# Kernel optimization log

Measured on AMD Instinct MI355X. Metric: run time of the kernel, lower is better.

The kernel has to match this reference:

```python
import jax, jax.numpy as jnp
import numpy as np

MARGIN = 0.25


def _cdist(x, y):
    # Euclidean distance matrix, same math as torch.cdist(p=2).
    # x: [M, D], y: [K, D] -> [M, K]
    sq = (
        jnp.sum(x * x, axis=1, keepdims=True)
        + jnp.sum(y * y, axis=1)[None, :]
        - 2.0 * (x @ y.T)
    )
    return jnp.sqrt(jnp.maximum(sq, 0.0))


def setup_inputs() -> dict:
    key = jax.random.key(0)
    k1, k2, k3 = jax.random.split(key, 3)
    B, P, N, D = 2048, 2048, 16, 128
    anchor = jax.random.normal(k1, (B, D), dtype=jnp.float32)
    positive = jax.random.normal(k2, (P, D), dtype=jnp.float32)
    negative = jax.random.normal(k3, (B, N, D), dtype=jnp.float32)
    return {"anchor": anchor, "positive": positive, "negative": negative}


def reference(anchor, positive, negative):
    B, N, D = negative.shape
    # hardest positive: max distance to any positive, per anchor -> [B]
    d_pos = _cdist(anchor, positive).max(axis=1)
    # Original torch code expands negatives across a redundant batch dim and
    # takes min over the flattened (B*B*N); per row this equals the GLOBAL min
    # over all anchor-negative pairs. Compute it without the duplication.
    neg_flat = negative.reshape(B * N, D)  # [B*N, D]
    d_neg = _cdist(anchor, neg_flat).min()  # scalar
    losses = jax.nn.relu(d_pos - d_neg + MARGIN)  # [B]
    return losses.mean()
```

## Files before the change

kernel.cpp:

```cpp
#include <hip/hip_runtime.h>
#include <hip/hip_bf16.h>

#define MARGIN_F 0.25f

#define B_ANCH 2048
#define P_POS  2048
#define N_NEG  32768
#define DDIM   128

typedef __attribute__((ext_vector_type(8))) short bf16x8;
typedef __attribute__((ext_vector_type(4))) float f32x4;

__device__ __forceinline__ short f2bf(float x) {
    __hip_bfloat16 h = __float2bfloat16(x);
    return *reinterpret_cast<short*>(&h);
}

__global__ __launch_bounds__(256) void prep_kernel(
    const float* __restrict__ anchor, const float* __restrict__ positive,
    const float* __restrict__ negative,
    short* __restrict__ pA, short* __restrict__ pP, short* __restrict__ pN,
    float* __restrict__ nA, float* __restrict__ nP, float* __restrict__ nN,
    unsigned* __restrict__ dposBits, unsigned* __restrict__ dnegBits)
{
    const int tile = blockIdx.x * 4 + (threadIdx.x >> 6);
    const int lane = threadIdx.x & 63;
    const int lm = lane & 15, lk = lane >> 4;

    const float* src; short* dst; float* nrm; int t;
    const int TA = B_ANCH / 16, TP = P_POS / 16;
    if (tile < TA) {
        src = anchor; dst = pA; nrm = nA; t = tile;
        if (lm == lane) dposBits[tile * 16 + lm] = 0u;
    } else if (tile < TA + TP) {
        src = positive; dst = pP; nrm = nP; t = tile - TA;
    } else {
        src = negative; dst = pN; nrm = nN; t = tile - TA - TP;
    }
    if (blockIdx.x == 0 && threadIdx.x == 0) *dnegBits = 0x7F800000u;

    const int row = t * 16 + lm;
    float ss = 0.f;
    #pragma unroll
    for (int s = 0; s < 4; ++s) {
        const float* sp = src + (size_t)row * DDIM + s * 32 + lk * 8;
        float4 v0 = *(const float4*)sp;
        float4 v1 = *(const float4*)(sp + 4);
        ss += v0.x*v0.x + v0.y*v0.y + v0.z*v0.z + v0.w*v0.w
            + v1.x*v1.x + v1.y*v1.y + v1.z*v1.z + v1.w*v1.w;
        bf16x8 o;
        o[0]=f2bf(v0.x); o[1]=f2bf(v0.y); o[2]=f2bf(v0.z); o[3]=f2bf(v0.w);
        o[4]=f2bf(v1.x); o[5]=f2bf(v1.y); o[6]=f2bf(v1.z); o[7]=f2bf(v1.w);
        *(bf16x8*)(dst + ((size_t)(t * 4 + s) * 64 + lane) * 8) = o;
    }
    ss += __shfl_xor(ss, 16);
    ss += __shfl_xor(ss, 32);
    if (lk == 0) nrm[row] = ss;
}

template<int MODE, int CT>
__device__ __forceinline__ void dist_tile(
    const bf16x8* __restrict__ Af, const bf16x8* __restrict__ Yf,
    const float* __restrict__ nA, const float* __restrict__ nY,
    int by, int bx,
    unsigned* __restrict__ dposBits, unsigned* __restrict__ dnegBits)
{
    const int wid  = threadIdx.x >> 6;
    const int lane = threadIdx.x & 63;
    const int lm = lane & 15, lk = lane >> 4;
    const int wr = wid >> 1, wc = wid & 1;
    const int rt0 = by * 8 + wr * 4;

    bf16x8 a[4][4];
    #pragma unroll
    for (int m = 0; m < 4; ++m)
        #pragma unroll
        for (int s = 0; s < 4; ++s)
            a[m][s] = Af[(size_t)((rt0 + m) * 4 + s) * 64 + lane];

    float red[4][4];
    #pragma unroll
    for (int m = 0; m < 4; ++m)
        #pragma unroll
        for (int r = 0; r < 4; ++r)
            red[m][r] = (MODE == 0) ? -3.4e38f : 3.4e38f;

    constexpr int G = CT * 4;

    bf16x8 b[3][4];
    float nyv[3];
    #pragma unroll
    for (int p = 0; p < 2 && p < G; ++p) {
        const int ctile = (bx * CT + (p >> 2)) * 8 + wc * 4 + (p & 3);
        #pragma unroll
        for (int s = 0; s < 4; ++s)
            b[p][s] = Yf[(size_t)(ctile * 4 + s) * 64 + lane];
        nyv[p] = nY[ctile * 16 + lm];
    }

    #pragma unroll
    for (int g = 0; g < G; ++g) {
        const int gp = g + 2;
        if (gp < G) {
            const int ctile = (bx * CT + (gp >> 2)) * 8 + wc * 4 + (gp & 3);
            #pragma unroll
            for (int s = 0; s < 4; ++s)
                b[gp % 3][s] = Yf[(size_t)(ctile * 4 + s) * 64 + lane];
            nyv[gp % 3] = nY[ctile * 16 + lm];
        }
        f32x4 acc[4];
        #pragma unroll
        for (int m = 0; m < 4; ++m) acc[m] = f32x4{0.f, 0.f, 0.f, 0.f};
        #pragma unroll
        for (int s = 0; s < 4; ++s)
            #pragma unroll
            for (int m = 0; m < 4; ++m)
                acc[m] = __builtin_amdgcn_mfma_f32_16x16x32_bf16(a[m][s], b[g % 3][s], acc[m], 0, 0, 0);
        const float ny = nyv[g % 3];
        #pragma unroll
        for (int m = 0; m < 4; ++m)
            #pragma unroll
            for (int r = 0; r < 4; ++r) {
                const float t = __builtin_fmaf(-2.f, acc[m][r], ny);
                red[m][r] = (MODE == 0) ? fmaxf(red[m][r], t) : fminf(red[m][r], t);
            }
    }

    float na[4][4];
    #pragma unroll
    for (int m = 0; m < 4; ++m)
        #pragma unroll
        for (int r = 0; r < 4; ++r)
            na[m][r] = nA[(rt0 + m) * 16 + 4 * lk + r];

    if (MODE == 0) {
        #pragma unroll
        for (int msk = 1; msk < 16; msk <<= 1)
            #pragma unroll
            for (int m = 0; m < 4; ++m)
                #pragma unroll
                for (int r = 0; r < 4; ++r)
                    red[m][r] = fmaxf(red[m][r], __shfl_xor(red[m][r], msk));
        if (lm == 0) {
            #pragma unroll
            for (int m = 0; m < 4; ++m)
                #pragma unroll
                for (int r = 0; r < 4; ++r) {
                    const float sq = fmaxf(na[m][r] + red[m][r], 0.f);
                    atomicMax(dposBits + ((rt0 + m) * 16 + 4 * lk + r),
                              __float_as_uint(sq));
                }
        }
    } else {
        float mn = 3.4e38f;
        #pragma unroll
        for (int m = 0; m < 4; ++m)
            #pragma unroll
            for (int r = 0; r < 4; ++r)
                mn = fminf(mn, na[m][r] + red[m][r]);
        mn = fmaxf(mn, 0.f);
        #pragma unroll
        for (int msk = 1; msk < 64; msk <<= 1) mn = fminf(mn, __shfl_xor(mn, msk));
        __shared__ float wmin[4];
        if (lane == 0) wmin[wid] = mn;
        __syncthreads();
        if (threadIdx.x == 0) {
            const float m2 = fminf(fminf(wmin[0], wmin[1]), fminf(wmin[2], wmin[3]));
            atomicMin(dnegBits, __float_as_uint(m2));
        }
    }
}

#define POS_BLOCKS ((P_POS / 128) * (B_ANCH / 128))
#define NEG_CT 8
#define NEG_BLOCKS ((N_NEG / (128 * NEG_CT)) * (B_ANCH / 128))

__global__ __launch_bounds__(256, 2) void fused_dist_kernel(
    const short* __restrict__ pA, const short* __restrict__ pP,
    const short* __restrict__ pN,
    const float* __restrict__ nA, const float* __restrict__ nP,
    const float* __restrict__ nN,
    unsigned* __restrict__ dposBits, unsigned* __restrict__ dnegBits)
{
    const int bid = blockIdx.x;
    if (bid < POS_BLOCKS) {
        dist_tile<0, 1>((const bf16x8*)pA, (const bf16x8*)pP, nA, nP,
                        bid >> 4, bid & 15, dposBits, dnegBits);
    } else {
        const int q = bid - POS_BLOCKS;
        dist_tile<1, NEG_CT>((const bf16x8*)pA, (const bf16x8*)pN, nA, nN,
                             q >> 5, q & 31, dposBits, dnegBits);
    }
}

__global__ __launch_bounds__(256) void finalize_kernel(
    const unsigned* __restrict__ dposBits, const unsigned* __restrict__ dnegBits,
    float* __restrict__ out)
{
    const float dneg = sqrtf(__uint_as_float(*dnegBits));
    float s = 0.f;
    for (int i = threadIdx.x; i < B_ANCH; i += 256) {
        float dp = sqrtf(__uint_as_float(dposBits[i]));
        s += fmaxf(dp - dneg + MARGIN_F, 0.f);
    }
    #pragma unroll
    for (int m = 1; m < 64; m <<= 1) s += __shfl_xor(s, m);
    __shared__ float ws[4];
    const int wid = threadIdx.x >> 6, lane = threadIdx.x & 63;
    if (lane == 0) ws[wid] = s;
    __syncthreads();
    if (threadIdx.x == 0)
        out[0] = (ws[0] + ws[1] + ws[2] + ws[3]) * (1.f / (float)B_ANCH);
}

extern "C" void kernel_launch(void* const* d_in, const int* in_sizes, int n_in,
                              void* d_out, int out_size, void* d_ws, size_t ws_size,
                              hipStream_t stream) {
    const float* anchor   = (const float*)d_in[0];
    const float* positive = (const float*)d_in[1];
    const float* negative = (const float*)d_in[2];
    float* out = (float*)d_out;

    char* ws = (char*)d_ws;
    size_t off = 0;
    auto alloc = [&](size_t bytes) { char* p = ws + off; off = (off + bytes + 255) & ~(size_t)255; return p; };

    short* pA = (short*)alloc((size_t)B_ANCH * DDIM * 2);
    short* pP = (short*)alloc((size_t)P_POS  * DDIM * 2);
    short* pN = (short*)alloc((size_t)N_NEG  * DDIM * 2);
    float* nA  = (float*)alloc((size_t)B_ANCH * 4);
    float* nP  = (float*)alloc((size_t)P_POS  * 4);
    float* nN  = (float*)alloc((size_t)N_NEG  * 4);
    unsigned* dposBits = (unsigned*)alloc((size_t)B_ANCH * 4);
    unsigned* dnegBits = (unsigned*)alloc(4);

    const int totalTiles = (B_ANCH + P_POS + N_NEG) / 16;
    prep_kernel<<<totalTiles / 4, 256, 0, stream>>>(
        anchor, positive, negative, pA, pP, pN, nA, nP, nN, dposBits, dnegBits);

    fused_dist_kernel<<<POS_BLOCKS + NEG_BLOCKS, 256, 0, stream>>>(
        pA, pP, pN, nA, nP, nN, dposBits, dnegBits);

    finalize_kernel<<<1, 256, 0, stream>>>(dposBits, dnegBits, out);
}
```

Baseline: 36.35 us.

## Fold -2 scale and norm into MFMA, fuse finalize via last-block counter

Prep now stores the anchor in bf16 pre-scaled by -2, and the MFMA accumulator starts at the column norm instead of zero. This removes the per-element FMA from the epilogue and leaves only a max/min. The reduction uses double-buffered accumulators, so the compare for the previous tile can overlap the current MFMAs. The separate finalize launch is dropped: the last block to finish, found through an atomic done-counter, computes the mean loss. This saves a kernel launch but adds a threadfence and an atomic to every block.

```diff
diff --git a/kernel.cpp b/kernel.cpp
--- a/kernel.cpp
+++ b/kernel.cpp
@@ -21,23 +21,27 @@
     const float* __restrict__ negative,
     short* __restrict__ pA, short* __restrict__ pP, short* __restrict__ pN,
     float* __restrict__ nA, float* __restrict__ nP, float* __restrict__ nN,
-    unsigned* __restrict__ dposBits, unsigned* __restrict__ dnegBits)
+    unsigned* __restrict__ dposBits, unsigned* __restrict__ dnegBits,
+    unsigned* __restrict__ doneCnt)
 {
     const int tile = blockIdx.x * 4 + (threadIdx.x >> 6);
     const int lane = threadIdx.x & 63;
     const int lm = lane & 15, lk = lane >> 4;
 
-    const float* src; short* dst; float* nrm; int t;
+    const float* src; short* dst; float* nrm; int t; float scl;
     const int TA = B_ANCH / 16, TP = P_POS / 16;
     if (tile < TA) {
-        src = anchor; dst = pA; nrm = nA; t = tile;
+        src = anchor; dst = pA; nrm = nA; t = tile; scl = -2.f;
         if (lm == lane) dposBits[tile * 16 + lm] = 0u;
     } else if (tile < TA + TP) {
-        src = positive; dst = pP; nrm = nP; t = tile - TA;
+        src = positive; dst = pP; nrm = nP; t = tile - TA; scl = 1.f;
     } else {
-        src = negative; dst = pN; nrm = nN; t = tile - TA - TP;
-    }
-    if (blockIdx.x == 0 && threadIdx.x == 0) *dnegBits = 0x7F800000u;
+        src = negative; dst = pN; nrm = nN; t = tile - TA - TP; scl = 1.f;
+    }
+    if (blockIdx.x == 0 && threadIdx.x == 0) {
+        *dnegBits = 0x7F800000u;
+        *doneCnt  = 0u;
+    }
 
     const int row = t * 16 + lm;
     float ss = 0.f;
@@ -49,8 +53,8 @@
         ss += v0.x*v0.x + v0.y*v0.y + v0.z*v0.z + v0.w*v0.w
             + v1.x*v1.x + v1.y*v1.y + v1.z*v1.z + v1.w*v1.w;
         bf16x8 o;
-        o[0]=f2bf(v0.x); o[1]=f2bf(v0.y); o[2]=f2bf(v0.z); o[3]=f2bf(v0.w);
-        o[4]=f2bf(v1.x); o[5]=f2bf(v1.y); o[6]=f2bf(v1.z); o[7]=f2bf(v1.w);
+        o[0]=f2bf(scl*v0.x); o[1]=f2bf(scl*v0.y); o[2]=f2bf(scl*v0.z); o[3]=f2bf(scl*v0.w);
+        o[4]=f2bf(scl*v1.x); o[5]=f2bf(scl*v1.y); o[6]=f2bf(scl*v1.z); o[7]=f2bf(scl*v1.w);
         *(bf16x8*)(dst + ((size_t)(t * 4 + s) * 64 + lane) * 8) = o;
     }
     ss += __shfl_xor(ss, 16);
@@ -98,32 +102,44 @@
         nyv[p] = nY[ctile * 16 + lm];
     }
 
+    f32x4 acc[2][4];
+
     #pragma unroll
     for (int g = 0; g < G; ++g) {
-        const int gp = g + 2;
-        if (gp < G) {
-            const int ctile = (bx * CT + (gp >> 2)) * 8 + wc * 4 + (gp & 3);
+        const int cb = g % 3;
+        const int ab = g & 1;
+        if (g + 2 < G) {
+            const int ctile = (bx * CT + ((g + 2) >> 2)) * 8 + wc * 4 + ((g + 2) & 3);
             #pragma unroll
             for (int s = 0; s < 4; ++s)
-                b[gp % 3][s] = Yf[(size_t)(ctile * 4 + s) * 64 + lane];
-            nyv[gp % 3] = nY[ctile * 16 + lm];
-        }
-        f32x4 acc[4];
-        #pragma unroll
-        for (int m = 0; m < 4; ++m) acc[m] = f32x4{0.f, 0.f, 0.f, 0.f};
+                b[(g + 2) % 3][s] = Yf[(size_t)(ctile * 4 + s) * 64 + lane];
+            nyv[(g + 2) % 3] = nY[ctile * 16 + lm];
+        }
+        const float ny = nyv[cb];
+        #pragma unroll
+        for (int m = 0; m < 4; ++m) acc[ab][m] = f32x4{ny, ny, ny, ny};
         #pragma unroll
         for (int s = 0; s < 4; ++s)
             #pragma unroll
             for (int m = 0; m < 4; ++m)
-                acc[m] = __builtin_amdgcn_mfma_f32_16x16x32_bf16(a[m][s], b[g % 3][s], acc[m], 0, 0, 0);
-        const float ny = nyv[g % 3];
+                acc[ab][m] = __builtin_amdgcn_mfma_f32_16x16x32_bf16(a[m][s], b[cb][s], acc[ab][m], 0, 0, 0);
+        if (g > 0) {
+            #pragma unroll
+            for (int m = 0; m < 4; ++m)
+                #pragma unroll
+                for (int r = 0; r < 4; ++r)
+                    red[m][r] = (MODE == 0) ? fmaxf(red[m][r], acc[ab ^ 1][m][r])
+                                            : fminf(red[m][r], acc[ab ^ 1][m][r]);
+        }
+    }
+    {
+        const int ab = (G - 1) & 1;
         #pragma unroll
         for (int m = 0; m < 4; ++m)
             #pragma unroll
-            for (int r = 0; r < 4; ++r) {
-                const float t = __builtin_fmaf(-2.f, acc[m][r], ny);
-                red[m][r] = (MODE == 0) ? fmaxf(red[m][r], t) : fminf(red[m][r], t);
-            }
+            for (int r = 0; r < 4; ++r)
+                red[m][r] = (MODE == 0) ? fmaxf(red[m][r], acc[ab][m][r])
+                                        : fminf(red[m][r], acc[ab][m][r]);
     }
 
     float na[4][4];
@@ -174,13 +190,15 @@
 #define POS_BLOCKS ((P_POS / 128) * (B_ANCH / 128))
 #define NEG_CT 8
 #define NEG_BLOCKS ((N_NEG / (128 * NEG_CT)) * (B_ANCH / 128))
+#define TOT_BLOCKS (POS_BLOCKS + NEG_BLOCKS)
 
 __global__ __launch_bounds__(256, 2) void fused_dist_kernel(
     const short* __restrict__ pA, const short* __restrict__ pP,
     const short* __restrict__ pN,
     const float* __restrict__ nA, const float* __restrict__ nP,
     const float* __restrict__ nN,
-    unsigned* __restrict__ dposBits, unsigned* __restrict__ dnegBits)
+    unsigned* __restrict__ dposBits, unsigned* __restrict__ dnegBits,
+    unsigned* __restrict__ doneCnt, float* __restrict__ out)
 {
     const int bid = blockIdx.x;
     if (bid < POS_BLOCKS) {
@@ -191,26 +209,29 @@
         dist_tile<1, NEG_CT>((const bf16x8*)pA, (const bf16x8*)pN, nA, nN,
                              q >> 5, q & 31, dposBits, dnegBits);
     }
-}
-
-__global__ __launch_bounds__(256) void finalize_kernel(
-    const unsigned* __restrict__ dposBits, const unsigned* __restrict__ dnegBits,
-    float* __restrict__ out)
-{
-    const float dneg = sqrtf(__uint_as_float(*dnegBits));
-    float s = 0.f;
-    for (int i = threadIdx.x; i < B_ANCH; i += 256) {
-        float dp = sqrtf(__uint_as_float(dposBits[i]));
-        s += fmaxf(dp - dneg + MARGIN_F, 0.f);
-    }
-    #pragma unroll
-    for (int m = 1; m < 64; m <<= 1) s += __shfl_xor(s, m);
-    __shared__ float ws[4];
-    const int wid = threadIdx.x >> 6, lane = threadIdx.x & 63;
-    if (lane == 0) ws[wid] = s;
+
+    __threadfence();
+    __shared__ unsigned lastFlag;
+    if (threadIdx.x == 0)
+        lastFlag = (atomicAdd(doneCnt, 1u) == TOT_BLOCKS - 1) ? 1u : 0u;
     __syncthreads();
-    if (threadIdx.x == 0)
-        out[0] = (ws[0] + ws[1] + ws[2] + ws[3]) * (1.f / (float)B_ANCH);
+    if (lastFlag) {
+        __threadfence();
+        const float dneg = sqrtf(__uint_as_float(atomicAdd(dnegBits, 0u)));
+        float s = 0.f;
+        for (int i = threadIdx.x; i < B_ANCH; i += 256) {
+            const float dp = sqrtf(__uint_as_float(atomicAdd(dposBits + i, 0u)));
+            s += fmaxf(dp - dneg + MARGIN_F, 0.f);
+        }
+        #pragma unroll
+        for (int m = 1; m < 64; m <<= 1) s += __shfl_xor(s, m);
+        __shared__ float ws4[4];
+        const int wid = threadIdx.x >> 6, lane = threadIdx.x & 63;
+        if (lane == 0) ws4[wid] = s;
+        __syncthreads();
+        if (threadIdx.x == 0)
+            out[0] = (ws4[0] + ws4[1] + ws4[2] + ws4[3]) * (1.f / (float)B_ANCH);
+    }
 }
 
 extern "C" void kernel_launch(void* const* d_in, const int* in_sizes, int n_in,
@@ -233,13 +254,13 @@
     float* nN  = (float*)alloc((size_t)N_NEG  * 4);
     unsigned* dposBits = (unsigned*)alloc((size_t)B_ANCH * 4);
     unsigned* dnegBits = (unsigned*)alloc(4);
+    unsigned* doneCnt  = (unsigned*)alloc(4);
 
     const int totalTiles = (B_ANCH + P_POS + N_NEG) / 16;
     prep_kernel<<<totalTiles / 4, 256, 0, stream>>>(
-        anchor, positive, negative, pA, pP, pN, nA, nP, nN, dposBits, dnegBits);
-
-    fused_dist_kernel<<<POS_BLOCKS + NEG_BLOCKS, 256, 0, stream>>>(
-        pA, pP, pN, nA, nP, nN, dposBits, dnegBits);
-
-    finalize_kernel<<<1, 256, 0, stream>>>(dposBits, dnegBits, out);
-}
+        anchor, positive, negative, pA, pP, pN, nA, nP, nN,
+        dposBits, dnegBits, doneCnt);
+
+    fused_dist_kernel<<<TOT_BLOCKS, 256, 0, stream>>>(
+        pA, pP, pN, nA, nP, nN, dposBits, dnegBits, doneCnt, out);
+}
```

New measurement: 79.32 us. 2.18x slower.
